# Optimization experiments

Hardware: AMD Instinct MI355X
Metric: run time of the kernel (lower is better)

Reference implementation:

```python
import jax, jax.numpy as jnp
import numpy as np

N_USER = 50000
N_ITEM = 100000
N_NODES = N_USER + N_ITEM  # 150000
EMB = 64
N_LAYERS = 3
NNZ = 2400000
BATCH = 4096
EPS = 1e-12  # F.normalize eps


def setup_inputs() -> dict:
    key = jax.random.key(0)
    ks = jax.random.split(key, 12)
    return {
        "users": jax.random.randint(ks[0], (BATCH,), 0, N_USER, dtype=jnp.int32),
        "pos_items": jax.random.randint(ks[1], (BATCH,), 0, N_ITEM, dtype=jnp.int32),
        "neg_items": jax.random.randint(ks[2], (BATCH,), 0, N_ITEM, dtype=jnp.int32),
        "adj_row": jax.random.randint(ks[3], (NNZ,), 0, N_NODES, dtype=jnp.int32),
        "adj_col": jax.random.randint(ks[4], (NNZ,), 0, N_NODES, dtype=jnp.int32),
        "adj_val": jax.random.uniform(ks[5], (NNZ,), dtype=jnp.float32),
        "user_emb": jax.random.normal(ks[6], (N_USER, EMB), dtype=jnp.float32) * 0.1,
        "item_emb": jax.random.normal(ks[7], (N_ITEM, EMB), dtype=jnp.float32) * 0.1,
        "W_gc": jax.random.normal(ks[8], (N_LAYERS, EMB, EMB), dtype=jnp.float32) * 0.1,
        "b_gc": jax.random.normal(ks[9], (N_LAYERS, 1, EMB), dtype=jnp.float32) * 0.1,
        "W_bi": jax.random.normal(ks[10], (N_LAYERS, EMB, EMB), dtype=jnp.float32) * 0.1,
        "b_bi": jax.random.normal(ks[11], (N_LAYERS, 1, EMB), dtype=jnp.float32) * 0.1,
    }


def reference(users, pos_items, neg_items, adj_row, adj_col, adj_val,
              user_emb, item_emb, W_gc, b_gc, W_bi, b_bi):
    # ego embeddings: concat user/item tables -> [N_NODES, EMB]
    ego = jnp.concatenate([user_emb, item_emb], axis=0)
    all_embs = [ego]
    for k in range(N_LAYERS):
        # sparse A_hat @ ego via gather + segment-sum over edges
        msgs = adj_val[:, None] * ego[adj_col]            # [NNZ, EMB]
        side = jax.ops.segment_sum(msgs, adj_row, num_segments=N_NODES)
        sum_emb = side @ W_gc[k] + b_gc[k]                # [N, EMB]
        bi_emb = (ego * side) @ W_bi[k] + b_bi[k]         # [N, EMB]
        ego = jax.nn.leaky_relu(sum_emb + bi_emb, negative_slope=0.2)
        # mess_dropout = 0 (eval mode) -> identity
        nrm = jnp.linalg.norm(ego, axis=1, keepdims=True)
        all_embs.append(ego / jnp.maximum(nrm, EPS))
    all_embs = jnp.concatenate(all_embs, axis=1)          # [N, EMB*(L+1)]
    u_g = all_embs[:N_USER]
    i_g = all_embs[N_USER:]
    return (u_g[users], i_g[pos_items], i_g[neg_items])
```

## Files before the change

### kernel.cpp

```cpp
#include <hip/hip_runtime.h>

typedef short bf16x8 __attribute__((ext_vector_type(8)));
typedef float f32x4  __attribute__((ext_vector_type(4)));

#define N_USER 50000
#define N_ITEM 100000
#define N_NODES 150000
#define EMB 64
#define NNZ 2400000
#define BATCH 4096
#define NSAMP (3 * BATCH)
#define NB 256
#define RPB 587
#define BS_GRID 256
#define EPB (NNZ / BS_GRID)

__device__ __forceinline__ unsigned int bf16_rne(float x) {
    unsigned int u = __float_as_uint(x);
    return (u + 0x7fffu + ((u >> 16) & 1u)) >> 16;
}
__device__ __forceinline__ float bflo(unsigned int u) { return __uint_as_float(u << 16); }
__device__ __forceinline__ float bfhi(unsigned int u) { return __uint_as_float(u & 0xffff0000u); }

__device__ __forceinline__ void fma8(float v, const uint4& x, float* acc) {
    acc[0] = fmaf(v, bflo(x.x), acc[0]); acc[1] = fmaf(v, bfhi(x.x), acc[1]);
    acc[2] = fmaf(v, bflo(x.y), acc[2]); acc[3] = fmaf(v, bfhi(x.y), acc[3]);
    acc[4] = fmaf(v, bflo(x.z), acc[4]); acc[5] = fmaf(v, bfhi(x.z), acc[5]);
    acc[6] = fmaf(v, bflo(x.w), acc[6]); acc[7] = fmaf(v, bfhi(x.w), acc[7]);
}
__device__ __forceinline__ uint4 pack8(const float* f) {
    return make_uint4((bf16_rne(f[1]) << 16) | bf16_rne(f[0]),
                      (bf16_rne(f[3]) << 16) | bf16_rne(f[2]),
                      (bf16_rne(f[5]) << 16) | bf16_rne(f[4]),
                      (bf16_rne(f[7]) << 16) | bf16_rne(f[6]));
}
__device__ __forceinline__ uint2 cvt2(const float4& v) {
    return make_uint2((bf16_rne(v.y) << 16) | bf16_rne(v.x),
                      (bf16_rne(v.w) << 16) | bf16_rne(v.z));
}

#define SEG_A (N_NODES * 4)
#define SEG_B (NSAMP * 16)
#define SEG_C (3 * 8192)
#define SEG_D 192
#define INIT_TOT (SEG_A + SEG_B + SEG_C + SEG_D + NSAMP)
#define INIT_BLOCKS ((INIT_TOT + 255) / 256)
__global__ __launch_bounds__(256) void binit(const int* __restrict__ rows,
                                             int* __restrict__ cnt,
                                             const float4* __restrict__ ue4,
                                             const float4* __restrict__ ie4,
                                             const int* __restrict__ users,
                                             const int* __restrict__ pos,
                                             const int* __restrict__ neg,
                                             uint2* __restrict__ ego_bf,
                                             float* __restrict__ out,
                                             int* __restrict__ samp,
                                             const float* __restrict__ Wgc,
                                             const float* __restrict__ Wbi,
                                             const float* __restrict__ bgc,
                                             const float* __restrict__ bbi,
                                             ushort* __restrict__ wbf,
                                             float* __restrict__ biasf) {
    __shared__ int h[NB];
    const int t = threadIdx.x;
    if (blockIdx.x < BS_GRID) {
        const int blk = blockIdx.x;
        h[t] = 0;
        __syncthreads();
        const int e0 = blk * EPB;
        for (int i = t; i < EPB; i += 256) atomicAdd(&h[rows[e0 + i] / RPB], 1);
        __syncthreads();
        cnt[t * BS_GRID + blk] = h[t];
        return;
    }
    int idx = (blockIdx.x - BS_GRID) * 256 + t;
    if (idx >= INIT_TOT) return;
    if (idx < SEG_A) {
        const int NU4 = N_USER * 16;
        int b4 = idx * 4;
        float4 a, b, c, d;
        if (b4 < NU4) { a = ue4[b4]; b = ue4[b4 + 1]; c = ue4[b4 + 2]; d = ue4[b4 + 3]; }
        else { int j = b4 - NU4; a = ie4[j]; b = ie4[j + 1]; c = ie4[j + 2]; d = ie4[j + 3]; }
        uint2 o0 = cvt2(a), o1 = cvt2(b), o2 = cvt2(c), o3 = cvt2(d);
        uint4* e4 = (uint4*)ego_bf;
        e4[idx * 2]     = make_uint4(o0.x, o0.y, o1.x, o1.y);
        e4[idx * 2 + 1] = make_uint4(o2.x, o2.y, o3.x, o3.y);
    } else if (idx < SEG_A + SEG_B) {
        int tt = idx - SEG_A;
        int r = tt >> 4, dq = tt & 15;
        int seg = r >> 12, bi = r & (BATCH - 1);
        int node = (seg == 0) ? users[bi] : N_USER + ((seg == 1) ? pos[bi] : neg[bi]);
        float4 v = (node < N_USER) ? ue4[node * 16 + dq] : ie4[(node - N_USER) * 16 + dq];
        ((float4*)out)[(size_t)r * 64 + dq] = v;
    } else if (idx < SEG_A + SEG_B + SEG_C) {
        int tt = idx - SEG_A - SEG_B;
        int l = tt >> 13, rem = tt & 8191;
        int k = rem >> 6, n = rem & 63;
        float w = (k < 64) ? Wgc[l * 4096 + k * 64 + n] : Wbi[l * 4096 + (k - 64) * 64 + n];
        wbf[l * 8704 + n * 136 + k] = (ushort)bf16_rne(w);
    } else if (idx < SEG_A + SEG_B + SEG_C + SEG_D) {
        int tt = idx - SEG_A - SEG_B - SEG_C;
        biasf[tt] = bgc[tt] + bbi[tt];
    } else {
        int tt = idx - SEG_A - SEG_B - SEG_C - SEG_D;
        int seg = tt >> 12, bi = tt & (BATCH - 1);
        samp[tt] = (seg == 0) ? users[bi] : N_USER + ((seg == 1) ? pos[bi] : neg[bi]);
    }
}

__global__ __launch_bounds__(1024) void scan64k(int* __restrict__ cnt) {
    __shared__ int s[1024];
    const int t = threadIdx.x;
    int loc[64], sum = 0;
#pragma unroll
    for (int i = 0; i < 64; ++i) { loc[i] = cnt[t * 64 + i]; sum += loc[i]; }
    s[t] = sum;
    for (int off = 1; off < 1024; off <<= 1) {
        __syncthreads();
        int add = (t >= off) ? s[t - off] : 0;
        __syncthreads();
        s[t] += add;
    }
    __syncthreads();
    int run = s[t] - sum;
#pragma unroll
    for (int i = 0; i < 64; ++i) { cnt[t * 64 + i] = run; run += loc[i]; }
}

__global__ __launch_bounds__(256) void bin_scatter(const int* __restrict__ rows,
                                                   const int* __restrict__ cols,
                                                   const float* __restrict__ vals,
                                                   const int* __restrict__ base,
                                                   int2* __restrict__ tmp_cv) {
    __shared__ int gbase[NB];
    __shared__ int cur[NB];
    const int t = threadIdx.x, blk = blockIdx.x;
    gbase[t] = base[t * BS_GRID + blk];
    cur[t] = 0;
    __syncthreads();
    const int e0 = blk * EPB;
    for (int i = t; i < EPB; i += 256) {
        int e = e0 + i;
        int r = rows[e];
        int b = r / RPB;
        int slot = atomicAdd(&cur[b], 1);
        unsigned vv = (__float_as_uint(vals[e]) & ~1023u) | (unsigned)(r - b * RPB);
        tmp_cv[gbase[b] + slot] = make_int2(cols[e], (int)vv);
    }
}

__global__ __launch_bounds__(256) void csr_from_bins(const int* __restrict__ base,
                                                     const int2* __restrict__ tmp_cv,
                                                     int2* __restrict__ ecv,
                                                     int* __restrict__ row_start) {
    __shared__ int rcnt[RPB];
    __shared__ int excl[RPB + 1];
    __shared__ int sc[256];
    const int b = blockIdx.x;
    const int row0 = b * RPB;
    const int t = threadIdx.x;
    const int beg = base[b * BS_GRID];
    const int end = (b == NB - 1) ? NNZ : base[(b + 1) * BS_GRID];

    for (int i = t; i < RPB; i += 256) rcnt[i] = 0;
    __syncthreads();
    for (int i = beg + t; i < end; i += 256) atomicAdd(&rcnt[tmp_cv[i].y & 1023], 1);
    __syncthreads();

    const int i0 = t * 3, i1 = i0 + 1, i2 = i0 + 2;
    int v0 = (i0 < RPB) ? rcnt[i0] : 0;
    int v1 = (i1 < RPB) ? rcnt[i1] : 0;
    int v2 = (i2 < RPB) ? rcnt[i2] : 0;
    int sum = v0 + v1 + v2;
    sc[t] = sum;
    for (int off = 1; off < 256; off <<= 1) {
        __syncthreads();
        int add = (t >= off) ? sc[t - off] : 0;
        __syncthreads();
        sc[t] += add;
    }
    __syncthreads();
    int ex = sc[t] - sum;
    if (i0 <= RPB) excl[i0] = ex;
    if (i1 <= RPB) excl[i1] = ex + v0;
    if (i2 <= RPB) excl[i2] = ex + v0 + v1;
    __syncthreads();

    int lim = N_NODES + 1 - row0;
    if (lim > RPB) lim = RPB;
    for (int i = t; i < lim; i += 256) row_start[row0 + i] = beg + excl[i];
    __syncthreads();
    for (int i = t; i < RPB; i += 256) rcnt[i] = excl[i];
    __syncthreads();
    for (int i = beg + t; i < end; i += 256) {
        int2 rec = tmp_cv[i];
        int r10 = rec.y & 1023;
        int dst = beg + atomicAdd(&rcnt[r10], 1);
        ecv[dst] = make_int2(rec.x, rec.y & ~1023);
    }
}

__global__ __launch_bounds__(256) void spmm_gemm(const int* __restrict__ row_start,
                                                 const int2* __restrict__ ecv,
                                                 const uint4* __restrict__ ego_bf,
                                                 const ushort* __restrict__ wbf,
                                                 const float* __restrict__ biasf,
                                                 ushort* __restrict__ ego_out,
                                                 float* __restrict__ inv_norm,
                                                 float* __restrict__ out,
                                                 const int* __restrict__ node_list,
                                                 int n_rows, int out_mode, int col0,
                                                 const ushort* __restrict__ g_ego,
                                                 const float* __restrict__ g_inv,
                                                 const int* __restrict__ g_samp,
                                                 int g_col0) {
    const int t = threadIdx.x;
    const int spmmBlocks = (n_rows + 31) >> 5;
    if ((int)blockIdx.x >= spmmBlocks) {
        int i = (blockIdx.x - spmmBlocks) * 256 + t;
        int r = i >> 6, d = i & 63;
        int node = g_samp[r];
        float v = __uint_as_float(((unsigned int)g_ego[(size_t)node * 64 + d]) << 16) * g_inv[node];
        out[(size_t)r * 256 + g_col0 + d] = v;
        return;
    }

    __shared__ ushort As[32][136];

    const int d8 = t & 7;
    const int rl = t >> 3;
    const int r = blockIdx.x * 32 + rl;
    const bool valid = (r < n_rows);
    const int node = valid ? (node_list ? node_list[r] : r) : 0;
    int s0 = 0, s1 = 0;
    if (valid) { s0 = row_start[node]; s1 = row_start[node + 1]; }
    const uint4 selfv = ego_bf[(size_t)node * 8 + d8];
    const int lbase = (t & 63) & 56;

    float acc[8] = {0.f, 0.f, 0.f, 0.f, 0.f, 0.f, 0.f, 0.f};
    for (int e0 = s0; e0 < s1; e0 += 8) {
        int2 m = make_int2(0, 0);
        if (e0 + d8 < s1) m = ecv[e0 + d8];
#pragma unroll
        for (int j = 0; j < 8; ++j) {
            int   c = __shfl(m.x, lbase + j);
            float v = __int_as_float(__shfl(m.y, lbase + j));
            const uint4 x = ego_bf[(size_t)c * 8 + d8];
            fma8(v, x, acc);
        }
    }
    float cs[8] = { bflo(selfv.x) * acc[0], bfhi(selfv.x) * acc[1],
                    bflo(selfv.y) * acc[2], bfhi(selfv.y) * acc[3],
                    bflo(selfv.z) * acc[4], bfhi(selfv.z) * acc[5],
                    bflo(selfv.w) * acc[6], bfhi(selfv.w) * acc[7] };
    *(uint4*)&As[rl][d8 * 8]      = pack8(acc);
    *(uint4*)&As[rl][64 + d8 * 8] = pack8(cs);
    __syncthreads();

    const int wv = t >> 6;
    if (wv >= 2) return;
    const int lane = t & 63;
    const int l15 = lane & 15, quad = lane >> 4;
    const bf16x8* wt8 = (const bf16x8*)wbf;
    const int arow = wv * 16 + l15;

    f32x4 C[4] = {{0,0,0,0}, {0,0,0,0}, {0,0,0,0}, {0,0,0,0}};
#pragma unroll
    for (int ks = 0; ks < 4; ++ks) {
        bf16x8 afr = *(const bf16x8*)&As[arow][(ks * 4 + quad) * 8];
        bf16x8 b0 = wt8[(0 * 16 + l15) * 17 + ks * 4 + quad];
        bf16x8 b1 = wt8[(1 * 16 + l15) * 17 + ks * 4 + quad];
        bf16x8 b2 = wt8[(2 * 16 + l15) * 17 + ks * 4 + quad];
        bf16x8 b3 = wt8[(3 * 16 + l15) * 17 + ks * 4 + quad];
        C[0] = __builtin_amdgcn_mfma_f32_16x16x32_bf16(afr, b0, C[0], 0, 0, 0);
        C[1] = __builtin_amdgcn_mfma_f32_16x16x32_bf16(afr, b1, C[1], 0, 0, 0);
        C[2] = __builtin_amdgcn_mfma_f32_16x16x32_bf16(afr, b2, C[2], 0, 0, 0);
        C[3] = __builtin_amdgcn_mfma_f32_16x16x32_bf16(afr, b3, C[3], 0, 0, 0);
    }

    float bias[4];
#pragma unroll
    for (int nt = 0; nt < 4; ++nt) bias[nt] = biasf[nt * 16 + l15];

    float x[4][4];
    float ss[4] = {0.f, 0.f, 0.f, 0.f};
#pragma unroll
    for (int nt = 0; nt < 4; ++nt)
#pragma unroll
        for (int rg = 0; rg < 4; ++rg) {
            float v = C[nt][rg] + bias[nt];
            v = (v >= 0.f) ? v : 0.2f * v;
            x[nt][rg] = v;
            ss[rg] = fmaf(v, v, ss[rg]);
        }
#pragma unroll
    for (int rg = 0; rg < 4; ++rg) {
        ss[rg] += __shfl_xor(ss[rg], 1);
        ss[rg] += __shfl_xor(ss[rg], 2);
        ss[rg] += __shfl_xor(ss[rg], 4);
        ss[rg] += __shfl_xor(ss[rg], 8);
    }
#pragma unroll
    for (int rg = 0; rg < 4; ++rg) {
        int row = blockIdx.x * 32 + wv * 16 + quad * 4 + rg;
        if (row >= n_rows) continue;
        float invr = 1.0f / fmaxf(sqrtf(ss[rg]), 1e-12f);
        if (out_mode) {
#pragma unroll
            for (int nt = 0; nt < 4; ++nt)
                out[(size_t)row * 256 + col0 + nt * 16 + l15] = x[nt][rg] * invr;
        } else {
#pragma unroll
            for (int nt = 0; nt < 4; ++nt)
                ego_out[(size_t)row * 64 + nt * 16 + l15] = (ushort)bf16_rne(x[nt][rg]);
            if (l15 == 0) inv_norm[row] = invr;
        }
    }
}

extern "C" void kernel_launch(void* const* d_in, const int* in_sizes, int n_in,
                              void* d_out, int out_size, void* d_ws, size_t ws_size,
                              hipStream_t stream) {
    const int* users = (const int*)d_in[0];
    const int* pos   = (const int*)d_in[1];
    const int* neg   = (const int*)d_in[2];
    const int* arow  = (const int*)d_in[3];
    const int* acol  = (const int*)d_in[4];
    const float* aval = (const float*)d_in[5];
    const float* ue   = (const float*)d_in[6];
    const float* ie   = (const float*)d_in[7];
    const float* Wgc  = (const float*)d_in[8];
    const float* bgc  = (const float*)d_in[9];
    const float* Wbi  = (const float*)d_in[10];
    const float* bbi  = (const float*)d_in[11];
    float* out = (float*)d_out;

    char* ws = (char*)d_ws;
    size_t o = 0;
    ushort* ego_a   = (ushort*)(ws + o); o += 19200000;
    ushort* ego_b   = (ushort*)(ws + o); o += 19200000;
    int2*   ecv     = (int2*)  (ws + o); o += (size_t)NNZ * 8;
    int2*   tmp_cv  = (int2*)  (ws + o); o += (size_t)NNZ * 8;
    int*    cnt     = (int*)   (ws + o); o += NB * BS_GRID * 4;
    int*    row_start = (int*) (ws + o); o += 600064;
    float*  inv_a     = (float*)(ws + o); o += 600064;
    float*  inv_b     = (float*)(ws + o); o += 600064;
    int*    samp      = (int*) (ws + o); o += 49152;
    ushort* wbf       = (ushort*)(ws + o); o += 52224;
    float*  biasf     = (float*)(ws + o); o += 768;

    const int gatherBlocks = (NSAMP * EMB) / 256;
    const int spmmN = (N_NODES + 31) / 32;
    const int spmmS = NSAMP / 32;

    binit<<<BS_GRID + INIT_BLOCKS, 256, 0, stream>>>(
        arow, cnt, (const float4*)ue, (const float4*)ie,
        users, pos, neg, (uint2*)ego_a, out, samp,
        Wgc, Wbi, bgc, bbi, wbf, biasf);
    scan64k<<<1, 1024, 0, stream>>>(cnt);
    bin_scatter<<<BS_GRID, 256, 0, stream>>>(arow, acol, aval, cnt, tmp_cv);
    csr_from_bins<<<NB, 256, 0, stream>>>(cnt, tmp_cv, ecv, row_start);

    spmm_gemm<<<spmmN, 256, 0, stream>>>(
        row_start, ecv, (const uint4*)ego_a, wbf, biasf,
        ego_b, inv_b, out, nullptr, N_NODES, 0, 0,
        nullptr, nullptr, nullptr, 0);

    spmm_gemm<<<spmmN + gatherBlocks, 256, 0, stream>>>(
        row_start, ecv, (const uint4*)ego_b, wbf + 8704, biasf + 64,
        ego_a, inv_a, out, nullptr, N_NODES, 0, 0,
        ego_b, inv_b, samp, 64);

    spmm_gemm<<<spmmS + gatherBlocks, 256, 0, stream>>>(
        row_start, ecv, (const uint4*)ego_a, wbf + 2 * 8704, biasf + 128,
        nullptr, nullptr, out, samp, NSAMP, 1, 192,
        ego_a, inv_a, samp, 128);
}
```

Measured before the change: 345.4 us.

## Widen CSR-build kernels to 1024 threads, vectorize scan, prefetch edge records in SpMM

Raises the block size of binit, bin_scatter and csr_from_bins from 256 to 1024 threads. This gives each block four times as many threads for the histogram and scatter loops, and lets csr_from_bins scan one row per thread without the excl staging array. scan64k now loads and stores its counts as int4 vectors. The SpMM edge loop software-prefetches the next 8 edge records before it processes the current ones, to hide ecv load latency. The risks are lower occupancy with 1024-thread blocks, heavier shared-atomic contention per block, and a changed scatter order within bins, which changes the floating-point summation order.

```diff
diff --git a/kernel.cpp b/kernel.cpp
--- a/kernel.cpp
+++ b/kernel.cpp
@@ -44,36 +44,36 @@
 #define SEG_C (3 * 8192)
 #define SEG_D 192
 #define INIT_TOT (SEG_A + SEG_B + SEG_C + SEG_D + NSAMP)
-#define INIT_BLOCKS ((INIT_TOT + 255) / 256)
-__global__ __launch_bounds__(256) void binit(const int* __restrict__ rows,
-                                             int* __restrict__ cnt,
-                                             const float4* __restrict__ ue4,
-                                             const float4* __restrict__ ie4,
-                                             const int* __restrict__ users,
-                                             const int* __restrict__ pos,
-                                             const int* __restrict__ neg,
-                                             uint2* __restrict__ ego_bf,
-                                             float* __restrict__ out,
-                                             int* __restrict__ samp,
-                                             const float* __restrict__ Wgc,
-                                             const float* __restrict__ Wbi,
-                                             const float* __restrict__ bgc,
-                                             const float* __restrict__ bbi,
-                                             ushort* __restrict__ wbf,
-                                             float* __restrict__ biasf) {
+#define INIT_BLOCKS ((INIT_TOT + 1023) / 1024)
+__global__ __launch_bounds__(1024) void binit(const int* __restrict__ rows,
+                                              int* __restrict__ cnt,
+                                              const float4* __restrict__ ue4,
+                                              const float4* __restrict__ ie4,
+                                              const int* __restrict__ users,
+                                              const int* __restrict__ pos,
+                                              const int* __restrict__ neg,
+                                              uint2* __restrict__ ego_bf,
+                                              float* __restrict__ out,
+                                              int* __restrict__ samp,
+                                              const float* __restrict__ Wgc,
+                                              const float* __restrict__ Wbi,
+                                              const float* __restrict__ bgc,
+                                              const float* __restrict__ bbi,
+                                              ushort* __restrict__ wbf,
+                                              float* __restrict__ biasf) {
     __shared__ int h[NB];
     const int t = threadIdx.x;
     if (blockIdx.x < BS_GRID) {
         const int blk = blockIdx.x;
-        h[t] = 0;
+        if (t < NB) h[t] = 0;
         __syncthreads();
         const int e0 = blk * EPB;
-        for (int i = t; i < EPB; i += 256) atomicAdd(&h[rows[e0 + i] / RPB], 1);
-        __syncthreads();
-        cnt[t * BS_GRID + blk] = h[t];
+        for (int i = t; i < EPB; i += 1024) atomicAdd(&h[rows[e0 + i] / RPB], 1);
+        __syncthreads();
+        if (t < NB) cnt[t * BS_GRID + blk] = h[t];
         return;
     }
-    int idx = (blockIdx.x - BS_GRID) * 256 + t;
+    int idx = (blockIdx.x - BS_GRID) * 1024 + t;
     if (idx >= INIT_TOT) return;
     if (idx < SEG_A) {
         const int NU4 = N_USER * 16;
@@ -111,9 +111,14 @@
 __global__ __launch_bounds__(1024) void scan64k(int* __restrict__ cnt) {
     __shared__ int s[1024];
     const int t = threadIdx.x;
-    int loc[64], sum = 0;
-#pragma unroll
-    for (int i = 0; i < 64; ++i) { loc[i] = cnt[t * 64 + i]; sum += loc[i]; }
+    int4 loc[16];
+    int sum = 0;
+    const int4* c4 = (const int4*)cnt;
+#pragma unroll
+    for (int i = 0; i < 16; ++i) {
+        loc[i] = c4[t * 16 + i];
+        sum += loc[i].x + loc[i].y + loc[i].z + loc[i].w;
+    }
     s[t] = sum;
     for (int off = 1; off < 1024; off <<= 1) {
         __syncthreads();
@@ -123,23 +128,31 @@
     }
     __syncthreads();
     int run = s[t] - sum;
-#pragma unroll
-    for (int i = 0; i < 64; ++i) { cnt[t * 64 + i] = run; run += loc[i]; }
-}
-
-__global__ __launch_bounds__(256) void bin_scatter(const int* __restrict__ rows,
-                                                   const int* __restrict__ cols,
-                                                   const float* __restrict__ vals,
-                                                   const int* __restrict__ base,
-                                                   int2* __restrict__ tmp_cv) {
+    int4* o4 = (int4*)cnt;
+#pragma unroll
+    for (int i = 0; i < 16; ++i) {
+        int4 v = loc[i];
+        int4 w;
+        w.x = run; run += v.x;
+        w.y = run; run += v.y;
+        w.z = run; run += v.z;
+        w.w = run; run += v.w;
+        o4[t * 16 + i] = w;
+    }
+}
+
+__global__ __launch_bounds__(1024) void bin_scatter(const int* __restrict__ rows,
+                                                    const int* __restrict__ cols,
+                                                    const float* __restrict__ vals,
+                                                    const int* __restrict__ base,
+                                                    int2* __restrict__ tmp_cv) {
     __shared__ int gbase[NB];
     __shared__ int cur[NB];
     const int t = threadIdx.x, blk = blockIdx.x;
-    gbase[t] = base[t * BS_GRID + blk];
-    cur[t] = 0;
+    if (t < NB) { gbase[t] = base[t * BS_GRID + blk]; cur[t] = 0; }
     __syncthreads();
     const int e0 = blk * EPB;
-    for (int i = t; i < EPB; i += 256) {
+    for (int i = t; i < EPB; i += 1024) {
         int e = e0 + i;
         int r = rows[e];
         int b = r / RPB;
@@ -149,50 +162,40 @@
     }
 }
 
-__global__ __launch_bounds__(256) void csr_from_bins(const int* __restrict__ base,
-                                                     const int2* __restrict__ tmp_cv,
-                                                     int2* __restrict__ ecv,
-                                                     int* __restrict__ row_start) {
+__global__ __launch_bounds__(1024) void csr_from_bins(const int* __restrict__ base,
+                                                      const int2* __restrict__ tmp_cv,
+                                                      int2* __restrict__ ecv,
+                                                      int* __restrict__ row_start) {
     __shared__ int rcnt[RPB];
-    __shared__ int excl[RPB + 1];
-    __shared__ int sc[256];
+    __shared__ int sc[1024];
     const int b = blockIdx.x;
     const int row0 = b * RPB;
     const int t = threadIdx.x;
     const int beg = base[b * BS_GRID];
     const int end = (b == NB - 1) ? NNZ : base[(b + 1) * BS_GRID];
 
-    for (int i = t; i < RPB; i += 256) rcnt[i] = 0;
-    __syncthreads();
-    for (int i = beg + t; i < end; i += 256) atomicAdd(&rcnt[tmp_cv[i].y & 1023], 1);
-    __syncthreads();
-
-    const int i0 = t * 3, i1 = i0 + 1, i2 = i0 + 2;
-    int v0 = (i0 < RPB) ? rcnt[i0] : 0;
-    int v1 = (i1 < RPB) ? rcnt[i1] : 0;
-    int v2 = (i2 < RPB) ? rcnt[i2] : 0;
-    int sum = v0 + v1 + v2;
-    sc[t] = sum;
-    for (int off = 1; off < 256; off <<= 1) {
+    if (t < RPB) rcnt[t] = 0;
+    __syncthreads();
+    for (int i = beg + t; i < end; i += 1024) atomicAdd(&rcnt[tmp_cv[i].y & 1023], 1);
+    __syncthreads();
+
+    int v = (t < RPB) ? rcnt[t] : 0;
+    sc[t] = v;
+    for (int off = 1; off < 1024; off <<= 1) {
         __syncthreads();
         int add = (t >= off) ? sc[t - off] : 0;
         __syncthreads();
         sc[t] += add;
     }
     __syncthreads();
-    int ex = sc[t] - sum;
-    if (i0 <= RPB) excl[i0] = ex;
-    if (i1 <= RPB) excl[i1] = ex + v0;
-    if (i2 <= RPB) excl[i2] = ex + v0 + v1;
-    __syncthreads();
+    int ex = sc[t] - v;
 
     int lim = N_NODES + 1 - row0;
     if (lim > RPB) lim = RPB;
-    for (int i = t; i < lim; i += 256) row_start[row0 + i] = beg + excl[i];
-    __syncthreads();
-    for (int i = t; i < RPB; i += 256) rcnt[i] = excl[i];
-    __syncthreads();
-    for (int i = beg + t; i < end; i += 256) {
+    if (t < lim) row_start[row0 + t] = beg + ex;
+    if (t < RPB) rcnt[t] = ex;
+    __syncthreads();
+    for (int i = beg + t; i < end; i += 1024) {
         int2 rec = tmp_cv[i];
         int r10 = rec.y & 1023;
         int dst = beg + atomicAdd(&rcnt[r10], 1);
@@ -238,9 +241,11 @@
     const int lbase = (t & 63) & 56;
 
     float acc[8] = {0.f, 0.f, 0.f, 0.f, 0.f, 0.f, 0.f, 0.f};
+    int2 m = make_int2(0, 0);
+    if (s0 + d8 < s1) m = ecv[s0 + d8];
     for (int e0 = s0; e0 < s1; e0 += 8) {
-        int2 m = make_int2(0, 0);
-        if (e0 + d8 < s1) m = ecv[e0 + d8];
+        int2 mn = make_int2(0, 0);
+        if (e0 + 8 + d8 < s1) mn = ecv[e0 + 8 + d8];
 #pragma unroll
         for (int j = 0; j < 8; ++j) {
             int   c = __shfl(m.x, lbase + j);
@@ -248,6 +253,7 @@
             const uint4 x = ego_bf[(size_t)c * 8 + d8];
             fma8(v, x, acc);
         }
+        m = mn;
     }
     float cs[8] = { bflo(selfv.x) * acc[0], bfhi(selfv.x) * acc[1],
                     bflo(selfv.y) * acc[2], bfhi(selfv.y) * acc[3],
@@ -353,13 +359,13 @@
     const int spmmN = (N_NODES + 31) / 32;
     const int spmmS = NSAMP / 32;
 
-    binit<<<BS_GRID + INIT_BLOCKS, 256, 0, stream>>>(
+    binit<<<BS_GRID + INIT_BLOCKS, 1024, 0, stream>>>(
         arow, cnt, (const float4*)ue, (const float4*)ie,
         users, pos, neg, (uint2*)ego_a, out, samp,
         Wgc, Wbi, bgc, bbi, wbf, biasf);
     scan64k<<<1, 1024, 0, stream>>>(cnt);
-    bin_scatter<<<BS_GRID, 256, 0, stream>>>(arow, acol, aval, cnt, tmp_cv);
-    csr_from_bins<<<NB, 256, 0, stream>>>(cnt, tmp_cv, ecv, row_start);
+    bin_scatter<<<BS_GRID, 1024, 0, stream>>>(arow, acol, aval, cnt, tmp_cv);
+    csr_from_bins<<<NB, 1024, 0, stream>>>(cnt, tmp_cv, ecv, row_start);
 
     spmm_gemm<<<spmmN, 256, 0, stream>>>(
         row_start, ecv, (const uint4*)ego_a, wbf, biasf,
```

Measured after the change: 316.4 us. 1.09x faster.
